# Optimization experiments

Measured on AMD Instinct MI355X. Metric: run time of the kernel, lower is better.

The kernel has to match this reference:

```python
import jax, jax.numpy as jnp
import numpy as np

EPS = 1e-3  # BatchNorm eps from the module

N_POINTS = 2_000_000
IN_CH = 10
OUT_CH = 32  # out_channels // 2 since last_layer=False
NUM_PILLARS = 50_000


def setup_inputs() -> dict:
    key = jax.random.key(0)
    k = jax.random.split(key, 7)
    inputs = jax.random.normal(k[0], (N_POINTS, IN_CH), dtype=jnp.float32)
    unq_inv = jax.random.randint(k[1], (N_POINTS,), 0, NUM_PILLARS, dtype=jnp.int32)
    W = jax.random.normal(k[2], (OUT_CH, IN_CH), dtype=jnp.float32) * 0.1
    gamma = jax.random.uniform(k[3], (OUT_CH,), dtype=jnp.float32, minval=0.5, maxval=1.5)
    beta = jax.random.normal(k[4], (OUT_CH,), dtype=jnp.float32) * 0.1
    running_mean = jax.random.normal(k[5], (OUT_CH,), dtype=jnp.float32) * 0.1
    running_var = jax.random.uniform(k[6], (OUT_CH,), dtype=jnp.float32, minval=0.5, maxval=1.5)
    return {"inputs": inputs, "unq_inv": unq_inv, "W": W, "gamma": gamma,
            "beta": beta, "running_mean": running_mean, "running_var": running_var,
            "num_out_inds": NUM_PILLARS}


def reference(inputs, unq_inv, W, gamma, beta, running_mean, running_var, num_out_inds):
    # Linear (bias=False): [N, in] @ [in, out] -> [N, out]
    x = inputs @ W.T
    # BatchNorm1d (inference-mode affine normalization)
    inv_std = jax.lax.rsqrt(running_var + EPS)
    x = (x - running_mean) * (inv_std * gamma) + beta
    x = jax.nn.relu(x)
    # scatter_max into a zeros-initialized buffer: empty segments stay 0,
    # and since x >= 0 post-ReLU, max-with-0 matches torch semantics exactly.
    x_max = jnp.maximum(
        jax.ops.segment_max(x, unq_inv, num_segments=num_out_inds), 0.0
    )  # [num_out_inds, OUT_CH]
    # gather per-pillar max back and concat (last_vfe=False branch)
    return jnp.concatenate([x, x_max[unq_inv]], axis=1)  # [N, 2*OUT_CH]
```

## Files before the change

### kernel.cpp

```cpp
#include <hip/hip_runtime.h>

#define N_IC 10
#define N_OC 32
#define PPB 128
#define BLK 256
#define PAD 11
#define NPIL 50000

typedef float f4 __attribute__((ext_vector_type(4)));

__global__ __launch_bounds__(BLK) void pfn_k1(
    const float* __restrict__ in, const int* __restrict__ unq,
    const float* __restrict__ W, const float* __restrict__ gamma,
    const float* __restrict__ beta, const float* __restrict__ rmean,
    const float* __restrict__ rvar,
    float* __restrict__ out, unsigned* __restrict__ pmax, int n)
{
    __shared__ float sW[N_OC][PAD];
    __shared__ float sB[N_OC];
    __shared__ float sIn[PPB][PAD];
    __shared__ int   sPil[PPB];

    const int t = threadIdx.x;
    if (t < N_OC) {
        float s = gamma[t] / sqrtf(rvar[t] + 1e-3f);
        sB[t] = fmaf(-rmean[t], s, beta[t]);
        #pragma unroll
        for (int k = 0; k < N_IC; ++k) sW[t][k] = W[t * N_IC + k] * s;
    }
    const long long base = (long long)blockIdx.x * PPB;
    for (int i = t; i < PPB * N_IC; i += BLK) {
        int p = i / N_IC;
        int k = i - p * N_IC;
        long long gp = base + p;
        sIn[p][k] = (gp < (long long)n) ? __builtin_nontemporal_load(&in[gp * N_IC + k]) : 0.f;
    }
    if (t < PPB) {
        long long gp = base + t;
        sPil[t] = (gp < (long long)n) ? unq[gp] : 0;
    }
    __syncthreads();

    const int o   = t & 31;
    const int sub = t >> 5;
    float w[N_IC];
    #pragma unroll
    for (int k = 0; k < N_IC; ++k) w[k] = sW[o][k];
    const float b = sB[o];

    #pragma unroll
    for (int it = 0; it < PPB; it += (BLK / 32)) {
        const int lp = it + sub;
        const long long gp = base + lp;
        if (gp < (long long)n) {
            float acc = b;
            #pragma unroll
            for (int k = 0; k < N_IC; ++k) acc = fmaf(sIn[lp][k], w[k], acc);
            float v = fmaxf(acc, 0.f);
            __builtin_nontemporal_store(v, &out[gp * 64 + o]);
            if (v > 0.f) {
                unsigned* addr = &pmax[(unsigned)sPil[lp] * N_OC + o];
                if (v > __uint_as_float(*addr))
                    atomicMax(addr, __float_as_uint(v));
            }
        }
    }
}

__global__ __launch_bounds__(BLK) void pfn_k2(
    const int* __restrict__ unq, const f4* __restrict__ pmax4,
    f4* __restrict__ out4, int n)
{
    long long tid = (long long)blockIdx.x * BLK + threadIdx.x;
    long long p = tid >> 3;
    int q = (int)(tid & 7);
    if (p < (long long)n) {
        int pil = unq[p];
        f4 v = pmax4[(long long)pil * 8 + q];
        __builtin_nontemporal_store(v, &out4[p * 16 + 8 + q]);
    }
}

extern "C" void kernel_launch(void* const* d_in, const int* in_sizes, int n_in,
                              void* d_out, int out_size, void* d_ws, size_t ws_size,
                              hipStream_t stream) {
    const float* in    = (const float*)d_in[0];
    const int*   unq   = (const int*)d_in[1];
    const float* W     = (const float*)d_in[2];
    const float* gamma = (const float*)d_in[3];
    const float* beta  = (const float*)d_in[4];
    const float* rmean = (const float*)d_in[5];
    const float* rvar  = (const float*)d_in[6];
    const int n = in_sizes[1];
    float* out = (float*)d_out;
    unsigned* pmax = (unsigned*)d_ws;

    size_t need = (size_t)NPIL * N_OC * sizeof(unsigned);
    hipMemsetAsync(d_ws, 0, need, stream);

    int g1 = (n + PPB - 1) / PPB;
    pfn_k1<<<g1, BLK, 0, stream>>>(in, unq, W, gamma, beta, rmean, rvar, out, pmax, n);

    long long threads2 = (long long)n * 8;
    int g2 = (int)((threads2 + BLK - 1) / BLK);
    pfn_k2<<<g2, BLK, 0, stream>>>(unq, (const f4*)d_ws, (f4*)out, n);
}
```

Measured before the change: 698.7 us.

## Compute four channels per thread with vector stores and use grid-stride gather kernel

Each thread in the first kernel now computes four adjacent output channels for one point. It writes them with a single 16-byte nontemporal store and reads the current pillar max as one vector load before issuing conditional atomics. This cuts the number of memory instructions and the per-channel pre-check loads, at the cost of more registers per thread. The gather kernel becomes a fixed 2048-block grid-stride loop, which reduces launch and block overhead.

```diff
diff --git a/kernel.cpp b/kernel.cpp
--- a/kernel.cpp
+++ b/kernel.cpp
@@ -16,7 +16,7 @@
     const float* __restrict__ rvar,
     float* __restrict__ out, unsigned* __restrict__ pmax, int n)
 {
-    __shared__ float sW[N_OC][PAD];
+    __shared__ float sW[N_OC][N_IC];
     __shared__ float sB[N_OC];
     __shared__ float sIn[PPB][PAD];
     __shared__ int   sPil[PPB];
@@ -41,27 +41,38 @@
     }
     __syncthreads();
 
-    const int o   = t & 31;
-    const int sub = t >> 5;
-    float w[N_IC];
+    const int qc = t & 7;
+    const int pr = t >> 3;
+    const int c0 = qc * 4;
+    float w[4][N_IC];
+    float b[4];
     #pragma unroll
-    for (int k = 0; k < N_IC; ++k) w[k] = sW[o][k];
-    const float b = sB[o];
+    for (int j = 0; j < 4; ++j) {
+        b[j] = sB[c0 + j];
+        #pragma unroll
+        for (int k = 0; k < N_IC; ++k) w[j][k] = sW[c0 + j][k];
+    }
 
     #pragma unroll
-    for (int it = 0; it < PPB; it += (BLK / 32)) {
-        const int lp = it + sub;
+    for (int it = 0; it < PPB; it += (BLK / 8)) {
+        const int lp = it + pr;
         const long long gp = base + lp;
         if (gp < (long long)n) {
-            float acc = b;
+            f4 v;
             #pragma unroll
-            for (int k = 0; k < N_IC; ++k) acc = fmaf(sIn[lp][k], w[k], acc);
-            float v = fmaxf(acc, 0.f);
-            __builtin_nontemporal_store(v, &out[gp * 64 + o]);
-            if (v > 0.f) {
-                unsigned* addr = &pmax[(unsigned)sPil[lp] * N_OC + o];
-                if (v > __uint_as_float(*addr))
-                    atomicMax(addr, __float_as_uint(v));
+            for (int j = 0; j < 4; ++j) {
+                float acc = b[j];
+                #pragma unroll
+                for (int k = 0; k < N_IC; ++k) acc = fmaf(sIn[lp][k], w[j][k], acc);
+                v[j] = fmaxf(acc, 0.f);
+            }
+            __builtin_nontemporal_store(v, (f4*)&out[gp * 64 + c0]);
+            const unsigned pil = (unsigned)sPil[lp];
+            f4 r = *(const f4*)&pmax[pil * N_OC + c0];
+            #pragma unroll
+            for (int j = 0; j < 4; ++j) {
+                if (v[j] > r[j])
+                    atomicMax(&pmax[pil * N_OC + c0 + j], __float_as_uint(v[j]));
             }
         }
     }
@@ -71,10 +82,12 @@
     const int* __restrict__ unq, const f4* __restrict__ pmax4,
     f4* __restrict__ out4, int n)
 {
-    long long tid = (long long)blockIdx.x * BLK + threadIdx.x;
-    long long p = tid >> 3;
-    int q = (int)(tid & 7);
-    if (p < (long long)n) {
+    const long long total  = (long long)n * 8;
+    const long long stride = (long long)gridDim.x * BLK;
+    for (long long tid = (long long)blockIdx.x * BLK + threadIdx.x;
+         tid < total; tid += stride) {
+        long long p = tid >> 3;
+        int q = (int)(tid & 7);
         int pil = unq[p];
         f4 v = pmax4[(long long)pil * 8 + q];
         __builtin_nontemporal_store(v, &out4[p * 16 + 8 + q]);
@@ -101,7 +114,5 @@
     int g1 = (n + PPB - 1) / PPB;
     pfn_k1<<<g1, BLK, 0, stream>>>(in, unq, W, gamma, beta, rmean, rvar, out, pmax, n);
 
-    long long threads2 = (long long)n * 8;
-    int g2 = (int)((threads2 + BLK - 1) / BLK);
-    pfn_k2<<<g2, BLK, 0, stream>>>(unq, (const f4*)d_ws, (f4*)out, n);
+    pfn_k2<<<2048, BLK, 0, stream>>>(unq, (const f4*)d_ws, (f4*)out, n);
 }
```

Measured after the change: 739.3 us. 1.06x slower.
